# Performance work log

Measured on AMD Instinct MI355X. Metric: run time of the kernel, lower is better.

Reference implementation:

```python
import jax, jax.numpy as jnp
import numpy as np

IH, IW, HEADS, DIM_HEAD = 32, 32, 8, 48
N = IH * IW
SCALE = DIM_HEAD ** -0.5
EPS = 1e-5


def _relative_index():
    # static precompute of relative distance indices, shape [N, N] int32
    yy, xx = np.meshgrid(np.arange(IH), np.arange(IW), indexing='ij')
    coords = np.stack([yy.ravel(), xx.ravel()])  # [2, N]
    rel = coords[:, :, None] - coords[:, None, :]  # [2, N, N]
    dist = np.ceil(np.sqrt(rel[0] ** 2 + rel[1] ** 2)).astype(np.int32)
    return jnp.asarray(dist)

REL_INDEX = _relative_index()


def _layernorm(x, w, b):
    mu = jnp.mean(x, axis=-1, keepdims=True)
    var = jnp.var(x, axis=-1, keepdims=True)
    return (x - mu) * jax.lax.rsqrt(var + EPS) * w + b


def setup_inputs() -> dict:
    key = jax.random.key(0)
    ks = jax.random.split(key, 8)
    d, inner, hid = 384, HEADS * DIM_HEAD, 1536
    return {
        'x': jax.random.normal(ks[0], (16, IH, IW, d), jnp.float32),
        'ln1_w': jnp.ones((d,), jnp.float32),
        'ln1_b': jnp.zeros((d,), jnp.float32),
        'w_qkv': jax.random.normal(ks[1], (d, 3 * inner), jnp.float32) * (d ** -0.5),
        'bias_table': jax.random.normal(ks[2], (45, HEADS), jnp.float32) * 0.02,
        'w_out': jax.random.normal(ks[3], (inner, d), jnp.float32) * (inner ** -0.5),
        'b_out': jnp.zeros((d,), jnp.float32),
        'ln2_w': jnp.ones((d,), jnp.float32),
        'ln2_b': jnp.zeros((d,), jnp.float32),
        'w1': jax.random.normal(ks[4], (d, hid), jnp.float32) * (d ** -0.5),
        'b1': jnp.zeros((hid,), jnp.float32),
        'w2': jax.random.normal(ks[5], (hid, d), jnp.float32) * (hid ** -0.5),
        'b2': jnp.zeros((d,), jnp.float32),
    }


def reference(x, ln1_w, ln1_b, w_qkv, bias_table, w_out, b_out,
              ln2_w, ln2_b, w1, b1, w2, b2):
    b = x.shape[0]
    xt = x.reshape(b, N, -1)  # b (ih iw) c

    # --- attention branch (PreNorm) ---
    h = _layernorm(xt, ln1_w, ln1_b)
    qkv = h @ w_qkv  # [b, N, 3*inner]
    q, k, v = jnp.split(qkv, 3, axis=-1)
    q = q.reshape(b, N, HEADS, DIM_HEAD).transpose(0, 2, 1, 3)
    k = k.reshape(b, N, HEADS, DIM_HEAD).transpose(0, 2, 1, 3)
    v = v.reshape(b, N, HEADS, DIM_HEAD).transpose(0, 2, 1, 3)
    dots = jnp.einsum('bhnd,bhmd->bhnm', q, k) * SCALE
    rel_bias = bias_table[REL_INDEX]  # [N, N, heads] gather
    dots = dots + rel_bias.transpose(2, 0, 1)[None]  # [1, h, N, N]
    attn = jax.nn.softmax(dots, axis=-1)
    out = jnp.einsum('bhnm,bhmd->bhnd', attn, v)
    out = out.transpose(0, 2, 1, 3).reshape(b, N, HEADS * DIM_HEAD)
    out = out @ w_out + b_out
    xt = xt + out

    # --- FFN branch (PreNorm) ---
    h = _layernorm(xt, ln2_w, ln2_b)
    h = jax.nn.gelu(h @ w1 + b1, approximate=False) @ w2 + b2
    xt = xt + h
    return xt.reshape(x.shape)
```

## Files before the change

kernel.cpp:

```cpp
#include <hip/hip_runtime.h>
#include <hip/hip_bf16.h>
#include <math.h>

typedef __bf16 bf16;
typedef __bf16 bf16x8 __attribute__((ext_vector_type(8)));
typedef __bf16 bf16x4 __attribute__((ext_vector_type(4)));
typedef __bf16 bf16x2 __attribute__((ext_vector_type(2)));
typedef float  f32x4  __attribute__((ext_vector_type(4)));

#define D_MODEL 384
#define HID     1536
#define NSEQ    1024
#define ROWS    16384
#define HEADS   8
#define DH      48
#define SCALE   0.14433756729740643f
#define MFIX    8.0f
#define BTAB_N  3969
#define BTAB_P  3972
#define KVT     4608
#define QP_BH   (NSEQ * DH)
#define KP_BH   (16 * KVT)

__device__ __forceinline__ void gload16(const void* g, void* l) {
    __builtin_amdgcn_global_load_lds((const __attribute__((address_space(1))) void*)g,
                                     (__attribute__((address_space(3))) void*)l, 16, 0, 0);
}

__device__ __forceinline__ float fast_gelu(float x) {
    float u = 0.7978845608f * fmaf(0.044715f * x * x, x, x);
    float e = __expf(2.f * u);
    float t = 1.f - 2.f * __builtin_amdgcn_rcpf(e + 1.f);
    return 0.5f * x * (1.f + t);
}

__global__ __launch_bounds__(256)
void bias_prep_kernel(const float* __restrict__ bias_table, float* __restrict__ Btab)
{
    int idx = blockIdx.x * 256 + threadIdx.x;
    if (idx >= BTAB_N) return;
    int dy = idx / 63 - 31, dx = idx % 63 - 31;
    int s2 = dy * dy + dx * dx;
    int r = (int)ceilf(sqrtf((float)s2));
    while (r * r < s2) ++r;
    while (r > 0 && (r - 1) * (r - 1) >= s2) --r;
#pragma unroll
    for (int h = 0; h < HEADS; ++h)
        Btab[h * BTAB_P + idx] = bias_table[r * HEADS + h] - MFIX;
}

__global__ __launch_bounds__(256)
void pack_init_kernel(bf16* __restrict__ Kp, bf16* __restrict__ Vp)
{
    const int bid = blockIdx.x, tid = threadIdx.x;
    if (bid < 512) {
        int row = bid * 256 + tid;
        bf16x8 z = {};
        bf16* p = Kp + (size_t)row * 72 + 48;
        *(bf16x8*)(p) = z;  *(bf16x8*)(p + 8) = z;  *(bf16x8*)(p + 16) = z;
    } else {
        int idx = (bid - 512) * 256 + tid;
        int tile = idx >> 4, rr = idx & 15;
        bf16 o = (bf16)1.f;
        bf16x8 ones = {o, o, o, o, o, o, o, o};
        bf16* p = Vp + (size_t)tile * KVT + (48 + rr) * 72;
#pragma unroll
        for (int c = 0; c < 9; ++c) *(bf16x8*)(p + c * 8) = ones;
    }
}

__global__ __launch_bounds__(256)
void wtrans_kernel(const float* __restrict__ in, bf16* __restrict__ out, int K, int N)
{
    __shared__ float T[64][65];
    const int k0 = blockIdx.y * 64, n0 = blockIdx.x * 64;
    const int rr = threadIdx.x >> 4, rc = threadIdx.x & 15;
#pragma unroll
    for (int i = 0; i < 4; ++i) {
        float4 v = *(const float4*)(in + (size_t)(k0 + rr + i * 16) * N + n0 + rc * 4);
        T[rr + i * 16][rc * 4 + 0] = v.x;  T[rr + i * 16][rc * 4 + 1] = v.y;
        T[rr + i * 16][rc * 4 + 2] = v.z;  T[rr + i * 16][rc * 4 + 3] = v.w;
    }
    __syncthreads();
#pragma unroll
    for (int i = 0; i < 4; ++i) {
        int n = rr + i * 16, kc = rc * 4;
        bf16x4 o;
        o[0] = (bf16)T[kc + 0][n];  o[1] = (bf16)T[kc + 1][n];
        o[2] = (bf16)T[kc + 2][n];  o[3] = (bf16)T[kc + 3][n];
        *(bf16x4*)(out + (size_t)(n0 + n) * K + k0 + kc) = o;
    }
}

__global__ __launch_bounds__(256)
void ln_kernel(const float* __restrict__ x, const float* __restrict__ w,
               const float* __restrict__ b, bf16* __restrict__ out)
{
    int row  = blockIdx.x * 4 + (threadIdx.x >> 6);
    int lane = threadIdx.x & 63;
    const float* xr = x + (size_t)row * D_MODEL;

    float2 v[3];
    float s = 0.f, ss = 0.f;
#pragma unroll
    for (int i = 0; i < 3; ++i) {
        v[i] = *(const float2*)(xr + lane * 2 + i * 128);
        s  += v[i].x + v[i].y;
        ss += v[i].x * v[i].x + v[i].y * v[i].y;
    }
#pragma unroll
    for (int off = 32; off; off >>= 1) {
        s  += __shfl_xor(s,  off);
        ss += __shfl_xor(ss, off);
    }
    float mu   = s * (1.f / D_MODEL);
    float var  = ss * (1.f / D_MODEL) - mu * mu;
    float rstd = rsqrtf(var + 1e-5f);

    bf16* orow = out + (size_t)row * D_MODEL;
#pragma unroll
    for (int i = 0; i < 3; ++i) {
        int c = lane * 2 + i * 128;
        float2 wv = *(const float2*)(w + c);
        float2 bv = *(const float2*)(b + c);
        bf16x2 o;
        o[0] = (bf16)((v[i].x - mu) * rstd * wv.x + bv.x);
        o[1] = (bf16)((v[i].y - mu) * rstd * wv.y + bv.y);
        *(bf16x2*)(orow + c) = o;
    }
}

template<int EPI, typename CT>
__global__ __launch_bounds__(256)
void gemm3_kernel(const bf16* __restrict__ A, const bf16* __restrict__ BT,
                  CT* __restrict__ C, const float* __restrict__ bias,
                  const float* __restrict__ res, int nxblk, int Nn, int K,
                  bf16* __restrict__ qp, bf16* __restrict__ kp, bf16* __restrict__ vp)
{
    __shared__ alignas(16) bf16 As[128][64];
    __shared__ alignas(16) bf16 Bs[128][64];

    const int bid  = blockIdx.x;
    const int xcd  = bid & 7;
    const int slot = bid >> 3;
    const int yy   = slot / nxblk;
    const int m0   = (yy * 8 + xcd) * 128;
    const int n0   = (slot - yy * nxblk) * 128;

    const int tid  = threadIdx.x;
    const int w    = tid >> 6;
    const int lane = tid & 63;
    const int quad = lane >> 4;
    const int l16  = lane & 15;

    const int srow = lane >> 3;
    const int scol = (lane & 7) * 8;

    f32x4 acc[4][4] = {};

    for (int kt = 0; kt < K; kt += 64) {
        __syncthreads();
#pragma unroll
        for (int c = 0; c < 4; ++c) {
            const int ch = w * 4 + c;
            gload16(A  + (size_t)(m0 + ch * 8 + srow) * K + kt + scol, &As[ch * 8][0]);
            gload16(BT + (size_t)(n0 + ch * 8 + srow) * K + kt + scol, &Bs[ch * 8][0]);
        }
        __syncthreads();

#pragma unroll
        for (int kk = 0; kk < 2; ++kk) {
            bf16x8 af[4], bfr[4];
#pragma unroll
            for (int mt = 0; mt < 4; ++mt)
                af[mt] = *(const bf16x8*)(&As[(w & 1) * 64 + mt * 16 + l16][kk * 32 + quad * 8]);
#pragma unroll
            for (int nt = 0; nt < 4; ++nt)
                bfr[nt] = *(const bf16x8*)(&Bs[(w >> 1) * 64 + nt * 16 + l16][kk * 32 + quad * 8]);
#pragma unroll
            for (int mt = 0; mt < 4; ++mt)
#pragma unroll
                for (int nt = 0; nt < 4; ++nt)
                    acc[mt][nt] = __builtin_amdgcn_mfma_f32_16x16x32_bf16(
                        af[mt], bfr[nt], acc[mt][nt], 0, 0, 0);
        }
    }

#pragma unroll
    for (int mt = 0; mt < 4; ++mt) {
#pragma unroll
        for (int nt = 0; nt < 4; ++nt) {
            const int c0 = n0 + (w >> 1) * 64 + nt * 16;
            const int c  = c0 + l16;
            float bi = (EPI == 1 || EPI == 2) ? bias[c] : 0.f;
#pragma unroll
            for (int r = 0; r < 4; ++r) {
                int row = m0 + (w & 1) * 64 + mt * 16 + quad * 4 + r;
                float v = acc[mt][nt][r] + bi;
                if (EPI == 1) {
                    v += res[(size_t)row * Nn + c];
                    C[(size_t)row * Nn + c] = (CT)v;
                } else if (EPI == 2) {
                    v = fast_gelu(v);
                    C[(size_t)row * Nn + c] = (CT)v;
                } else {
                    int b   = row >> 10, seq = row & 1023;
                    if (c0 < 384) {
                        int h = c / 48, d = c - h * 48;
                        qp[(size_t)(b * 8 + h) * QP_BH + seq * 48 + d] = (bf16)(v * SCALE);
                    } else if (c0 < 768) {
                        int ck = c - 384;
                        int h = ck / 48, d = ck - h * 48;
                        kp[(size_t)(b * 8 + h) * KP_BH + (seq >> 6) * KVT
                           + (seq & 63) * 72 + d] = (bf16)v;
                    } else {
                        int cv = c - 768;
                        int h = cv / 48, d = cv - h * 48;
                        vp[(size_t)(b * 8 + h) * KP_BH + (seq >> 6) * KVT
                           + d * 72 + (seq & 63)] = (bf16)v;
                    }
                }
            }
        }
    }
}

__global__ __launch_bounds__(512)
void attn_kernel(const bf16* __restrict__ Qp, const bf16* __restrict__ Kp,
                 const bf16* __restrict__ Vp, const float* __restrict__ Btab,
                 bf16* __restrict__ out)
{
    __shared__ alignas(16) bf16 Ks[64][72];
    __shared__ alignas(16) bf16 Vs[64][72];
    __shared__ alignas(16) bf16 Ps[8][2][16][72];
    __shared__ alignas(16) float B2f[BTAB_P];

    const int bid  = blockIdx.x;
    const int xcd  = bid & 7;
    const int slot = bid >> 3;
    const int qc   = slot & 3;
    const int bh   = (slot >> 2) * 8 + xcd;
    const int q0   = qc * 256;
    const int tid  = threadIdx.x;
    const int wave = tid >> 6;
    const int lane = tid & 63;
    const int quad = lane >> 4;
    const int l16  = lane & 15;
    const int b    = bh >> 3, h = bh & 7;

    {
        const char* src = (const char*)(Btab + h * BTAB_P);
#pragma unroll
        for (int it = 0; it < 2; ++it) {
            int off = it * 8192 + tid * 16;
            if (off < BTAB_P * 4)
                gload16(src + off, (char*)B2f + it * 8192 + wave * 1024);
        }
    }

    bf16x8 qf0[2], qf1[2];
    int pi[2];
#pragma unroll
    for (int s = 0; s < 2; ++s) {
        int qrow = q0 + s * 128 + wave * 16 + l16;
        const bf16* qptr = Qp + (size_t)bh * QP_BH + qrow * 48;
        qf0[s] = *(const bf16x8*)(qptr + quad * 8);
#pragma unroll
        for (int c = 0; c < 8; ++c) qf1[s][c] = (bf16)0.f;
        if (quad < 2) qf1[s] = *(const bf16x8*)(qptr + 32 + quad * 8);
        pi[s] = (qrow >> 5) * 63 + (qrow & 31) + 31 * 63 + 31;
    }

    f32x4 o_acc[2][4] = {};

    for (int t = 0; t < 16; ++t) {
        const int n0 = t * 64;
        const bf16* kbase = Kp + (size_t)(bh * 16 + t) * KVT;
        const bf16* vbase = Vp + (size_t)(bh * 16 + t) * KVT;
        __syncthreads();
        for (int i = wave; i < 9; i += 8) {
            gload16(kbase + i * 512 + lane * 8, (bf16*)Ks + i * 512);
            gload16(vbase + i * 512 + lane * 8, (bf16*)Vs + i * 512);
        }
        __syncthreads();

        f32x4 sa[2][4] = {};
#pragma unroll
        for (int nt = 0; nt < 4; ++nt) {
            bf16x8 a0 = *(const bf16x8*)(&Ks[nt * 16 + l16][quad * 8]);
            bf16x8 a1 = *(const bf16x8*)(&Ks[nt * 16 + l16][32 + quad * 8]);
#pragma unroll
            for (int s = 0; s < 2; ++s) {
                sa[s][nt] = __builtin_amdgcn_mfma_f32_16x16x32_bf16(a0, qf0[s], sa[s][nt], 0, 0, 0);
                sa[s][nt] = __builtin_amdgcn_mfma_f32_16x16x32_bf16(a1, qf1[s], sa[s][nt], 0, 0, 0);
            }
        }

#pragma unroll
        for (int s = 0; s < 2; ++s)
#pragma unroll
            for (int nt = 0; nt < 4; ++nt) {
                const int j0 = n0 + nt * 16 + quad * 4;
                const int ib = pi[s] - ((j0 >> 5) * 63 + (j0 & 31));
                bf16x4 pk;
#pragma unroll
                for (int r = 0; r < 4; ++r)
                    pk[r] = (bf16)__expf(sa[s][nt][r] + B2f[ib - r]);
                *(bf16x4*)(&Ps[wave][s][l16][nt * 16 + quad * 4]) = pk;
            }

#pragma unroll
        for (int kk = 0; kk < 2; ++kk) {
            bf16x8 vf[4];
#pragma unroll
            for (int d = 0; d < 4; ++d)
                vf[d] = *(const bf16x8*)(&Vs[d * 16 + l16][kk * 32 + quad * 8]);
#pragma unroll
            for (int s = 0; s < 2; ++s) {
                bf16x8 pf = *(const bf16x8*)(&Ps[wave][s][l16][kk * 32 + quad * 8]);
#pragma unroll
                for (int d = 0; d < 4; ++d)
                    o_acc[s][d] = __builtin_amdgcn_mfma_f32_16x16x32_bf16(
                        pf, vf[d], o_acc[s][d], 0, 0, 0);
            }
        }
    }

#pragma unroll
    for (int s = 0; s < 2; ++s)
#pragma unroll
        for (int r = 0; r < 4; ++r) {
            float inv = 1.f / o_acc[s][3][r];
            int row = q0 + s * 128 + wave * 16 + quad * 4 + r;
            bf16* orow = out + ((size_t)b * NSEQ + row) * D_MODEL + h * DH;
#pragma unroll
            for (int d = 0; d < 3; ++d)
                orow[d * 16 + l16] = (bf16)(o_acc[s][d][r] * inv);
        }
}

extern "C" void kernel_launch(void* const* d_in, const int* in_sizes, int n_in,
                              void* d_out, int out_size, void* d_ws, size_t ws_size,
                              hipStream_t stream)
{
    const float* x          = (const float*)d_in[0];
    const float* ln1_w      = (const float*)d_in[1];
    const float* ln1_b      = (const float*)d_in[2];
    const float* w_qkv      = (const float*)d_in[3];
    const float* bias_table = (const float*)d_in[4];
    const float* w_out      = (const float*)d_in[5];
    const float* b_out      = (const float*)d_in[6];
    const float* ln2_w      = (const float*)d_in[7];
    const float* ln2_b      = (const float*)d_in[8];
    const float* w1         = (const float*)d_in[9];
    const float* b1         = (const float*)d_in[10];
    const float* w2         = (const float*)d_in[11];
    const float* b2         = (const float*)d_in[12];
    float* out = (float*)d_out;

    bf16* regA  = (bf16*)d_ws;
    bf16* Qpack = regA;
    bf16* Kpack = regA + 6291456;
    bf16* Vpack = regA + 15728640;
    bf16* regB  = regA + (size_t)ROWS * HID;
    bf16* wqkvT = regB + (size_t)ROWS * D_MODEL;
    bf16* woutT = wqkvT + 1152 * 384;
    bf16* w1T   = woutT + 384 * 384;
    bf16* w2T   = w1T + 1536 * 384;
    float* Btab = (float*)(w2T + 384 * 1536);
    float* x1   = out;

    bias_prep_kernel<<<(BTAB_N + 255) / 256, 256, 0, stream>>>(bias_table, Btab);
    pack_init_kernel<<<640, 256, 0, stream>>>(Kpack, Vpack);
    wtrans_kernel<<<dim3(1152 / 64, 384 / 64), 256, 0, stream>>>(w_qkv, wqkvT, 384, 1152);
    wtrans_kernel<<<dim3(384 / 64, 384 / 64), 256, 0, stream>>>(w_out, woutT, 384, 384);
    wtrans_kernel<<<dim3(1536 / 64, 384 / 64), 256, 0, stream>>>(w1, w1T, 384, 1536);
    wtrans_kernel<<<dim3(384 / 64, 1536 / 64), 256, 0, stream>>>(w2, w2T, 1536, 384);

    ln_kernel<<<ROWS / 4, 256, 0, stream>>>(x, ln1_w, ln1_b, regB);
    gemm3_kernel<3, bf16><<<(1152 / 128) * (ROWS / 128), 256, 0, stream>>>(
        regB, wqkvT, (bf16*)nullptr, nullptr, nullptr, 1152 / 128, 1152, D_MODEL,
        Qpack, Kpack, Vpack);
    attn_kernel<<<512, 512, 0, stream>>>(Qpack, Kpack, Vpack, Btab, regB);
    gemm3_kernel<1, float><<<(D_MODEL / 128) * (ROWS / 128), 256, 0, stream>>>(
        regB, woutT, x1, b_out, x, D_MODEL / 128, D_MODEL, D_MODEL,
        nullptr, nullptr, nullptr);
    ln_kernel<<<ROWS / 4, 256, 0, stream>>>(x1, ln2_w, ln2_b, regB);
    gemm3_kernel<2, bf16><<<(HID / 128) * (ROWS / 128), 256, 0, stream>>>(
        regB, w1T, regA, b1, nullptr, HID / 128, HID, D_MODEL,
        nullptr, nullptr, nullptr);
    gemm3_kernel<1, float><<<(D_MODEL / 128) * (ROWS / 128), 256, 0, stream>>>(
        regA, w2T, out, b2, x1, D_MODEL / 128, D_MODEL, HID,
        nullptr, nullptr, nullptr);
}
```

Before: 319.8 us.

## Fuse prep kernels with LN1, halve bias table, double attention KV tile

```diff
diff --git a/kernel.cpp b/kernel.cpp
--- a/kernel.cpp
+++ b/kernel.cpp
@@ -16,8 +16,7 @@
 #define DH      48
 #define SCALE   0.14433756729740643f
 #define MFIX    8.0f
-#define BTAB_N  3969
-#define BTAB_P  3972
+#define BT2_N   2016
 #define KVT     4608
 #define QP_BH   (NSEQ * DH)
 #define KP_BH   (16 * KVT)
@@ -34,46 +33,11 @@
     return 0.5f * x * (1.f + t);
 }
 
-__global__ __launch_bounds__(256)
-void bias_prep_kernel(const float* __restrict__ bias_table, float* __restrict__ Btab)
-{
-    int idx = blockIdx.x * 256 + threadIdx.x;
-    if (idx >= BTAB_N) return;
-    int dy = idx / 63 - 31, dx = idx % 63 - 31;
-    int s2 = dy * dy + dx * dx;
-    int r = (int)ceilf(sqrtf((float)s2));
-    while (r * r < s2) ++r;
-    while (r > 0 && (r - 1) * (r - 1) >= s2) --r;
-#pragma unroll
-    for (int h = 0; h < HEADS; ++h)
-        Btab[h * BTAB_P + idx] = bias_table[r * HEADS + h] - MFIX;
-}
-
-__global__ __launch_bounds__(256)
-void pack_init_kernel(bf16* __restrict__ Kp, bf16* __restrict__ Vp)
-{
-    const int bid = blockIdx.x, tid = threadIdx.x;
-    if (bid < 512) {
-        int row = bid * 256 + tid;
-        bf16x8 z = {};
-        bf16* p = Kp + (size_t)row * 72 + 48;
-        *(bf16x8*)(p) = z;  *(bf16x8*)(p + 8) = z;  *(bf16x8*)(p + 16) = z;
-    } else {
-        int idx = (bid - 512) * 256 + tid;
-        int tile = idx >> 4, rr = idx & 15;
-        bf16 o = (bf16)1.f;
-        bf16x8 ones = {o, o, o, o, o, o, o, o};
-        bf16* p = Vp + (size_t)tile * KVT + (48 + rr) * 72;
-#pragma unroll
-        for (int c = 0; c < 9; ++c) *(bf16x8*)(p + c * 8) = ones;
-    }
-}
-
-__global__ __launch_bounds__(256)
-void wtrans_kernel(const float* __restrict__ in, bf16* __restrict__ out, int K, int N)
-{
-    __shared__ float T[64][65];
-    const int k0 = blockIdx.y * 64, n0 = blockIdx.x * 64;
+__device__ __forceinline__ void wtrans_body(const float* __restrict__ in,
+                                            bf16* __restrict__ out, int K, int N,
+                                            int bx, int by, float (*T)[65])
+{
+    const int k0 = by * 64, n0 = bx * 64;
     const int rr = threadIdx.x >> 4, rc = threadIdx.x & 15;
 #pragma unroll
     for (int i = 0; i < 4; ++i) {
@@ -92,11 +56,12 @@
     }
 }
 
-__global__ __launch_bounds__(256)
-void ln_kernel(const float* __restrict__ x, const float* __restrict__ w,
-               const float* __restrict__ b, bf16* __restrict__ out)
-{
-    int row  = blockIdx.x * 4 + (threadIdx.x >> 6);
+__device__ __forceinline__ void ln_body(const float* __restrict__ x,
+                                        const float* __restrict__ w,
+                                        const float* __restrict__ b,
+                                        bf16* __restrict__ out, int blk)
+{
+    int row  = blk * 4 + ((int)threadIdx.x >> 6);
     int lane = threadIdx.x & 63;
     const float* xr = x + (size_t)row * D_MODEL;
 
@@ -128,6 +93,66 @@
         o[1] = (bf16)((v[i].y - mu) * rstd * wv.y + bv.y);
         *(bf16x2*)(orow + c) = o;
     }
+}
+
+__global__ __launch_bounds__(256)
+void prep_kernel(const float* __restrict__ w_qkv, const float* __restrict__ w_out,
+                 const float* __restrict__ w1, const float* __restrict__ w2,
+                 bf16* __restrict__ wqkvT, bf16* __restrict__ woutT,
+                 bf16* __restrict__ w1T, bf16* __restrict__ w2T,
+                 bf16* __restrict__ Kp, bf16* __restrict__ Vp,
+                 const float* __restrict__ bias_table, float* __restrict__ Btab,
+                 const float* __restrict__ x, const float* __restrict__ ln1_w,
+                 const float* __restrict__ ln1_b, bf16* __restrict__ regB)
+{
+    __shared__ float T[64][65];
+    const int bid = blockIdx.x, tid = threadIdx.x;
+
+    if (bid < 432) {
+        const float* in; bf16* outp; int K, N, nx, local;
+        if (bid < 108)      { in = w_qkv; outp = wqkvT; K = 384;  N = 1152; local = bid;       nx = 18; }
+        else if (bid < 144) { in = w_out; outp = woutT; K = 384;  N = 384;  local = bid - 108; nx = 6;  }
+        else if (bid < 288) { in = w1;    outp = w1T;   K = 384;  N = 1536; local = bid - 144; nx = 24; }
+        else                { in = w2;    outp = w2T;   K = 1536; N = 384;  local = bid - 288; nx = 6;  }
+        wtrans_body(in, outp, K, N, local % nx, local / nx, T);
+    } else if (bid < 1072) {
+        const int pb = bid - 432;
+        if (pb < 512) {
+            int row = pb * 256 + tid;
+            bf16x8 z = {};
+            bf16* p = Kp + (size_t)row * 72 + 48;
+            *(bf16x8*)(p) = z;  *(bf16x8*)(p + 8) = z;  *(bf16x8*)(p + 16) = z;
+        } else {
+            int idx = (pb - 512) * 256 + tid;
+            int tile = idx >> 4, rr = idx & 15;
+            bf16 o = (bf16)1.f;
+            bf16x8 ones = {o, o, o, o, o, o, o, o};
+            bf16* p = Vp + (size_t)tile * KVT + (48 + rr) * 72;
+#pragma unroll
+            for (int c = 0; c < 9; ++c) *(bf16x8*)(p + c * 8) = ones;
+        }
+    } else if (bid < 1080) {
+        int idx = (bid - 1072) * 256 + tid;
+        if (idx < BT2_N) {
+            int dy = idx / 63, dx = idx % 63 - 31;
+            int s2 = dy * dy + dx * dx;
+            int r = (int)ceilf(sqrtf((float)s2));
+            while (r * r < s2) ++r;
+            while (r > 0 && (r - 1) * (r - 1) >= s2) --r;
+#pragma unroll
+            for (int h = 0; h < HEADS; ++h)
+                Btab[h * BT2_N + idx] = bias_table[r * HEADS + h] - MFIX;
+        }
+    } else {
+        ln_body(x, ln1_w, ln1_b, regB, bid - 1080);
+    }
+}
+
+__global__ __launch_bounds__(256)
+void ln_kernel(const float* __restrict__ x, const float* __restrict__ w,
+               const float* __restrict__ b, bf16* __restrict__ out)
+{
+    ln_body(x, w, b, out, blockIdx.x);
 }
 
 template<int EPI, typename CT>
@@ -230,10 +255,10 @@
                  const bf16* __restrict__ Vp, const float* __restrict__ Btab,
                  bf16* __restrict__ out)
 {
-    __shared__ alignas(16) bf16 Ks[64][72];
-    __shared__ alignas(16) bf16 Vs[64][72];
+    __shared__ alignas(16) bf16 Ks[128][72];
+    __shared__ alignas(16) bf16 Vs[2][64][72];
     __shared__ alignas(16) bf16 Ps[8][2][16][72];
-    __shared__ alignas(16) float B2f[BTAB_P];
+    __shared__ alignas(16) float B2f[BT2_N];
 
     const int bid  = blockIdx.x;
     const int xcd  = bid & 7;
@@ -249,17 +274,14 @@
     const int b    = bh >> 3, h = bh & 7;
 
     {
-        const char* src = (const char*)(Btab + h * BTAB_P);
-#pragma unroll
-        for (int it = 0; it < 2; ++it) {
-            int off = it * 8192 + tid * 16;
-            if (off < BTAB_P * 4)
-                gload16(src + off, (char*)B2f + it * 8192 + wave * 1024);
-        }
+        const char* src = (const char*)(Btab + (size_t)h * BT2_N);
+        int off = tid * 16;
+        if (off < BT2_N * 4)
+            gload16(src + off, (char*)B2f + wave * 1024);
     }
 
     bf16x8 qf0[2], qf1[2];
-    int pi[2];
+    int qy[2], qxp[2];
 #pragma unroll
     for (int s = 0; s < 2; ++s) {
         int qrow = q0 + s * 128 + wave * 16 + l16;
@@ -268,60 +290,67 @@
 #pragma unroll
         for (int c = 0; c < 8; ++c) qf1[s][c] = (bf16)0.f;
         if (quad < 2) qf1[s] = *(const bf16x8*)(qptr + 32 + quad * 8);
-        pi[s] = (qrow >> 5) * 63 + (qrow & 31) + 31 * 63 + 31;
+        qy[s]  = qrow >> 5;
+        qxp[s] = (qrow & 31) + 31;
     }
 
     f32x4 o_acc[2][4] = {};
 
-    for (int t = 0; t < 16; ++t) {
-        const int n0 = t * 64;
-        const bf16* kbase = Kp + (size_t)(bh * 16 + t) * KVT;
-        const bf16* vbase = Vp + (size_t)(bh * 16 + t) * KVT;
+    for (int t = 0; t < 8; ++t) {
+        const bf16* kbase = Kp + (size_t)(bh * 16 + 2 * t) * KVT;
+        const bf16* vbase = Vp + (size_t)(bh * 16 + 2 * t) * KVT;
         __syncthreads();
-        for (int i = wave; i < 9; i += 8) {
+        for (int i = wave; i < 18; i += 8) {
             gload16(kbase + i * 512 + lane * 8, (bf16*)Ks + i * 512);
-            gload16(vbase + i * 512 + lane * 8, (bf16*)Vs + i * 512);
+            gload16(vbase + i * 512 + lane * 8, (bf16*)&Vs[0][0][0] + i * 512);
         }
         __syncthreads();
 
-        f32x4 sa[2][4] = {};
-#pragma unroll
-        for (int nt = 0; nt < 4; ++nt) {
-            bf16x8 a0 = *(const bf16x8*)(&Ks[nt * 16 + l16][quad * 8]);
-            bf16x8 a1 = *(const bf16x8*)(&Ks[nt * 16 + l16][32 + quad * 8]);
-#pragma unroll
-            for (int s = 0; s < 2; ++s) {
-                sa[s][nt] = __builtin_amdgcn_mfma_f32_16x16x32_bf16(a0, qf0[s], sa[s][nt], 0, 0, 0);
-                sa[s][nt] = __builtin_amdgcn_mfma_f32_16x16x32_bf16(a1, qf1[s], sa[s][nt], 0, 0, 0);
+#pragma unroll
+        for (int hf = 0; hf < 2; ++hf) {
+            const int n0 = t * 128 + hf * 64;
+
+            f32x4 sa[2][4] = {};
+#pragma unroll
+            for (int nt = 0; nt < 4; ++nt) {
+                bf16x8 a0 = *(const bf16x8*)(&Ks[hf * 64 + nt * 16 + l16][quad * 8]);
+                bf16x8 a1 = *(const bf16x8*)(&Ks[hf * 64 + nt * 16 + l16][32 + quad * 8]);
+#pragma unroll
+                for (int s = 0; s < 2; ++s) {
+                    sa[s][nt] = __builtin_amdgcn_mfma_f32_16x16x32_bf16(a0, qf0[s], sa[s][nt], 0, 0, 0);
+                    sa[s][nt] = __builtin_amdgcn_mfma_f32_16x16x32_bf16(a1, qf1[s], sa[s][nt], 0, 0, 0);
+                }
             }
-        }
-
-#pragma unroll
-        for (int s = 0; s < 2; ++s)
-#pragma unroll
-            for (int nt = 0; nt < 4; ++nt) {
-                const int j0 = n0 + nt * 16 + quad * 4;
-                const int ib = pi[s] - ((j0 >> 5) * 63 + (j0 & 31));
-                bf16x4 pk;
-#pragma unroll
-                for (int r = 0; r < 4; ++r)
-                    pk[r] = (bf16)__expf(sa[s][nt][r] + B2f[ib - r]);
-                *(bf16x4*)(&Ps[wave][s][l16][nt * 16 + quad * 4]) = pk;
-            }
-
-#pragma unroll
-        for (int kk = 0; kk < 2; ++kk) {
-            bf16x8 vf[4];
-#pragma unroll
-            for (int d = 0; d < 4; ++d)
-                vf[d] = *(const bf16x8*)(&Vs[d * 16 + l16][kk * 32 + quad * 8]);
-#pragma unroll
-            for (int s = 0; s < 2; ++s) {
-                bf16x8 pf = *(const bf16x8*)(&Ps[wave][s][l16][kk * 32 + quad * 8]);
+
+#pragma unroll
+            for (int s = 0; s < 2; ++s)
+#pragma unroll
+                for (int nt = 0; nt < 4; ++nt) {
+                    const int j0 = n0 + nt * 16 + quad * 4;
+                    int dy  = qy[s] - (j0 >> 5);
+                    int iay = dy < 0 ? -dy : dy;
+                    const int ib0 = iay * 63 + qxp[s] - (j0 & 31);
+                    bf16x4 pk;
+#pragma unroll
+                    for (int r = 0; r < 4; ++r)
+                        pk[r] = (bf16)__expf(sa[s][nt][r] + B2f[ib0 - r]);
+                    *(bf16x4*)(&Ps[wave][s][l16][nt * 16 + quad * 4]) = pk;
+                }
+
+#pragma unroll
+            for (int kk = 0; kk < 2; ++kk) {
+                bf16x8 vf[4];
 #pragma unroll
                 for (int d = 0; d < 4; ++d)
-                    o_acc[s][d] = __builtin_amdgcn_mfma_f32_16x16x32_bf16(
-                        pf, vf[d], o_acc[s][d], 0, 0, 0);
+                    vf[d] = *(const bf16x8*)(&Vs[hf][d * 16 + l16][kk * 32 + quad * 8]);
+#pragma unroll
+                for (int s = 0; s < 2; ++s) {
+                    bf16x8 pf = *(const bf16x8*)(&Ps[wave][s][l16][kk * 32 + quad * 8]);
+#pragma unroll
+                    for (int d = 0; d < 4; ++d)
+                        o_acc[s][d] = __builtin_amdgcn_mfma_f32_16x16x32_bf16(
+                            pf, vf[d], o_acc[s][d], 0, 0, 0);
+                }
             }
         }
     }
@@ -370,14 +399,9 @@
     float* Btab = (float*)(w2T + 384 * 1536);
     float* x1   = out;
 
-    bias_prep_kernel<<<(BTAB_N + 255) / 256, 256, 0, stream>>>(bias_table, Btab);
-    pack_init_kernel<<<640, 256, 0, stream>>>(Kpack, Vpack);
-    wtrans_kernel<<<dim3(1152 / 64, 384 / 64), 256, 0, stream>>>(w_qkv, wqkvT, 384, 1152);
-    wtrans_kernel<<<dim3(384 / 64, 384 / 64), 256, 0, stream>>>(w_out, woutT, 384, 384);
-    wtrans_kernel<<<dim3(1536 / 64, 384 / 64), 256, 0, stream>>>(w1, w1T, 384, 1536);
-    wtrans_kernel<<<dim3(384 / 64, 1536 / 64), 256, 0, stream>>>(w2, w2T, 1536, 384);
-
-    ln_kernel<<<ROWS / 4, 256, 0, stream>>>(x, ln1_w, ln1_b, regB);
+    prep_kernel<<<5176, 256, 0, stream>>>(
+        w_qkv, w_out, w1, w2, wqkvT, woutT, w1T, w2T,
+        Kpack, Vpack, bias_table, Btab, x, ln1_w, ln1_b, regB);
     gemm3_kernel<3, bf16><<<(1152 / 128) * (ROWS / 128), 256, 0, stream>>>(
         regB, wqkvT, (bf16*)nullptr, nullptr, nullptr, 1152 / 128, 1152, D_MODEL,
         Qpack, Kpack, Vpack);
```

Result: faster. 307.9 us (-3.7%).
